# Kernel optimization log

Hardware: AMD Instinct MI355X
Metric: run time of the kernel (lower is better)

The kernel has to match this reference:

```python
import jax, jax.numpy as jnp
import numpy as np

NUM_PTS = 4
N_OFF = 4


def inverse_sigmoid(x, eps=1e-5):
    x = jnp.clip(x, 0.0, 1.0)
    return jnp.log(jnp.clip(x, eps, None) / jnp.clip(1.0 - x, eps, None))


def uniform_flat_indices(T, H, W, n):
    # torch: linspace(hop/2, D-1-hop/2, n).round().long(), meshed over (t,h,w)
    def ax(D):
        hop = D / n
        return jnp.round(jnp.linspace(hop / 2.0, D - 1.0 - hop / 2.0, n)).astype(jnp.int32)
    ti, hi, wi = ax(T), ax(H), ax(W)
    return ((ti[:, None, None] * H + hi[None, :, None]) * W + wi[None, None, :]).reshape(-1)


def _normalized_thw(idx, T, H, W):
    wn = (idx % W).astype(jnp.float32) / (W - 1)
    hn = ((idx // W) % H).astype(jnp.float32) / (H - 1)
    tn = (idx // (W * H)).astype(jnp.float32) / (T - 1)
    return jnp.stack([tn, hn, wn], axis=-1)


def grid_sample_3d(inp, grid):
    # Matches torch F.grid_sample 5D, bilinear, padding zeros, align_corners=False.
    # inp: (N,C,D,H,W); grid: (N,Do,Ho,Wo,3) with grid[...,0]=x->W, 1=y->H, 2=z->D
    N, C, D, H, W = inp.shape
    Do, Ho, Wo = grid.shape[1:4]
    P = Do * Ho * Wo
    g = grid.reshape(N, P, 3)
    ix = ((g[..., 0] + 1.0) * W - 1.0) * 0.5
    iy = ((g[..., 1] + 1.0) * H - 1.0) * 0.5
    iz = ((g[..., 2] + 1.0) * D - 1.0) * 0.5
    x0 = jnp.floor(ix); y0 = jnp.floor(iy); z0 = jnp.floor(iz)
    fx = ix - x0; fy = iy - y0; fz = iz - z0
    x0i = x0.astype(jnp.int32); y0i = y0.astype(jnp.int32); z0i = z0.astype(jnp.int32)
    inp_flat = inp.reshape(N, C, D * H * W)
    out = jnp.zeros((N, C, P), inp.dtype)
    for dz in (0, 1):
        for dy in (0, 1):
            for dx in (0, 1):
                xi = x0i + dx; yi = y0i + dy; zi = z0i + dz
                w = (fx if dx else 1.0 - fx) * (fy if dy else 1.0 - fy) * (fz if dz else 1.0 - fz)
                valid = (xi >= 0) & (xi < W) & (yi >= 0) & (yi < H) & (zi >= 0) & (zi < D)
                flat = (jnp.clip(zi, 0, D - 1) * H + jnp.clip(yi, 0, H - 1)) * W + jnp.clip(xi, 0, W - 1)
                vals = jnp.take_along_axis(inp_flat, jnp.broadcast_to(flat[:, None, :], (N, C, P)), axis=2)
                out = out + vals * (w * valid.astype(inp.dtype))[:, None, :]
    return out.reshape(N, C, Do, Ho, Wo)


def forward(features, pos, W1, b1, W2, b2, Wn, bn, Wl, bl, Woff, boff, Ww, bw, gamma, beta):
    B, C, T, H, Wd, L = features.shape
    THW = T * H * Wd
    No = N_OFF
    N = NUM_PTS ** 3
    d = C // No
    BLNo = B * L * No

    flat = uniform_flat_indices(T, H, Wd, NUM_PTS)                    # (N,)
    ind_pts = jnp.broadcast_to(flat[None, None, :], (B, L, N))

    feats_l = jnp.transpose(features, (0, 5, 2, 3, 4, 1)).reshape(B, L, THW, C)
    pos_l = jnp.transpose(pos, (0, 5, 2, 3, 4, 1)).reshape(B, L, THW, C)
    sampled_pts = feats_l[:, :, flat, :]                              # (B,L,N,C)
    sampled_pos = pos_l[:, :, flat, :]
    glob = jnp.transpose(jnp.mean(features, axis=(2, 3, 4)), (0, 2, 1))  # (B,L,C)
    glob = jnp.broadcast_to(glob[:, :, None, :], (B, L, N, C))

    off_src = jnp.concatenate([sampled_pts, sampled_pos, glob], axis=-1)
    off_src = jax.nn.relu(off_src @ W1 + b1)
    off_src = jax.nn.relu(off_src @ W2 + b2)                          # (B,L,N,C)

    nxt = off_src @ Wn + bn                                           # (B,L,N,3)
    w_l = jax.nn.softmax(off_src @ Wl + bl, axis=-1)                  # (B,L,N,L)

    osr = off_src.reshape(B, L, N, No, d).transpose(0, 1, 3, 2, 4).reshape(BLNo, N, d)
    offset = osr @ Woff + boff                                        # (BLNo,N,3)
    w_o = jax.nn.softmax(osr @ Ww + bw, axis=-1)[..., 1:]             # (BLNo,N,1)

    # --- build flow field: identity grid with sampled coords scattered in ---
    idx = jnp.broadcast_to(ind_pts[:, :, None, :], (B, L, No, N)).reshape(BLNo, N)
    thw = _normalized_thw(idx, T, H, Wd)
    samp = jax.nn.sigmoid(inverse_sigmoid(thw) + offset) * 2.0 - 1.0  # (BLNo,N,3)
    mesh = jnp.stack(jnp.meshgrid(jnp.linspace(-1.0, 1.0, T), jnp.linspace(-1.0, 1.0, H), jnp.linspace(-1.0, 1.0, Wd), indexing='ij'), axis=-1).reshape(THW, 3)
    base = jnp.broadcast_to(mesh[None], (BLNo, THW, 3))
    bI = jnp.arange(BLNo)[:, None]
    flow = base.at[bI, idx].set(samp).reshape(BLNo, T, H, Wd, 3)

    feats_rep = jnp.transpose(features, (0, 5, 1, 2, 3, 4))           # (B,L,C,T,H,W)
    feats_rep = jnp.broadcast_to(feats_rep[:, :, None], (B, L, No, C, T, H, Wd)).reshape(BLNo, C, T, H, Wd)
    sf = grid_sample_3d(feats_rep, flow)                              # (BLNo,C,T,H,W)
    sf = jnp.transpose(sf, (0, 2, 3, 4, 1))                           # (BLNo,T,H,W,C)

    wo_full = jnp.zeros((BLNo, THW, 1), features.dtype).at[bI, idx].set(w_o).reshape(BLNo, T, H, Wd, 1)
    wsf = (sf * wo_full).reshape(B, L, No, T, H, Wd, C).sum(axis=2)   # (B,L,T,H,W,C)
    feats2 = features + jnp.transpose(wsf, (0, 5, 2, 3, 4, 1))        # (B,C,T,H,W,L)

    # level weights scattered then summed over target-level axis l
    bI2 = jnp.arange(B)[:, None, None]
    lI2 = jnp.arange(L)[None, :, None]
    wl_full = jnp.zeros((B, L, THW, L), features.dtype).at[bI2, lI2, ind_pts].set(w_l)
    wl_sum = wl_full.sum(axis=-1).reshape(B, L, T, H, Wd)             # (B,L,T,H,W)
    feats3 = feats2 * jnp.transpose(wl_sum, (0, 2, 3, 4, 1))[:, None] # broadcast over C

    # LayerNorm over channel dim (transpose(1,-1) in torch)
    x = jnp.transpose(feats3, (0, 5, 2, 3, 4, 1))                     # (B,L,T,H,W,C)
    mu = jnp.mean(x, axis=-1, keepdims=True)
    var = jnp.var(x, axis=-1, keepdims=True)
    xn = (x - mu) * jax.lax.rsqrt(var + 1e-5) * gamma + beta
    feats_out = jnp.transpose(xn, (0, 5, 2, 3, 4, 1))

    # offset_adder -> next flattened indices
    thw2 = _normalized_thw(ind_pts, T, H, Wd)
    disp = jax.nn.sigmoid(inverse_sigmoid(thw2) + nxt)
    scale = jnp.array([T - 1, H - 1, Wd - 1], jnp.float32)
    di = jnp.round(disp * scale).astype(jnp.int32)
    next_ind = H * Wd * di[..., 0] + Wd * di[..., 1] + di[..., 2]
    return feats_out, next_ind


def setup_inputs():
    key = jax.random.key(0)
    ks = jax.random.split(key, 10)
    B, C, T, H, W, L = 1, 256, 8, 32, 32, 4
    s = 0.02
    d = C // N_OFF
    return {
        'features': jax.random.normal(ks[0], (B, C, T, H, W, L), jnp.float32),
        'pos': jax.random.normal(ks[1], (B, C, T, H, W, L), jnp.float32),
        'W1': jax.random.normal(ks[2], (3 * C, C), jnp.float32) * s,
        'b1': jnp.zeros((C,), jnp.float32),
        'W2': jax.random.normal(ks[3], (C, C), jnp.float32) * s,
        'b2': jnp.zeros((C,), jnp.float32),
        'Wn': jax.random.normal(ks[4], (C, 3), jnp.float32) * s,
        'bn': jnp.zeros((3,), jnp.float32),
        'Wl': jax.random.normal(ks[5], (C, L), jnp.float32) * s,
        'bl': jnp.zeros((L,), jnp.float32),
        'Woff': jax.random.normal(ks[6], (d, 3), jnp.float32) * s,
        'boff': jnp.zeros((3,), jnp.float32),
        'Ww': jax.random.normal(ks[7], (d, 2), jnp.float32) * s,
        'bw': jnp.zeros((2,), jnp.float32),
        'gamma': jnp.ones((C,), jnp.float32),
        'beta': jnp.zeros((C,), jnp.float32),
    }


def reference(features, pos, W1, b1, W2, b2, Wn, bn, Wl, bl, Woff, boff, Ww, bw, gamma, beta):
    return forward(features, pos, W1, b1, W2, b2, Wn, bn, Wl, bl, Woff, boff, Ww, bw, gamma, beta)
```

## Files before the change

kernel.cpp:

```cpp
#include <hip/hip_runtime.h>
#include <math.h>

#define CDIM 256
#define TDIM 8
#define HDIM 32
#define WDIM 32
#define LDIM 4
#define THW 8192
#define CSTR 32768
#define NS 64
#define OUT0_SIZE 8388608

__device__ __constant__ int c_ti[4] = {1, 3, 4, 6};
__device__ __constant__ int c_hw[4] = {4, 12, 19, 27};

__device__ __forceinline__ float sigm(float x) { return 1.f / (1.f + expf(-x)); }

__device__ __forceinline__ float wave_sum64(float x) {
#pragma unroll
    for (int s = 32; s > 0; s >>= 1) x += __shfl_xor(x, s, 64);
    return x;
}

__global__ void __launch_bounds__(256)
k_fill_part(const float* __restrict__ feat, const float* __restrict__ beta,
            float* __restrict__ out, float4* __restrict__ partF) {
    int c = blockIdx.x >> 3, part = blockIdx.x & 7;
    float bv = beta[c];
    float4 bf = make_float4(bv, bv, bv, bv);
    const float4* f = (const float4*)(feat + (size_t)c * CSTR) + part * 1024;
    float4* o = (float4*)(out + (size_t)c * CSTR) + part * 1024;
    float4 a = make_float4(0.f, 0.f, 0.f, 0.f);
#pragma unroll
    for (int it = 0; it < 4; ++it) {
        int i = it * 256 + threadIdx.x;
        float4 v = f[i];
        o[i] = bf;
        a.x += v.x; a.y += v.y; a.z += v.z; a.w += v.w;
    }
#pragma unroll
    for (int s = 32; s > 0; s >>= 1) {
        a.x += __shfl_xor(a.x, s, 64);
        a.y += __shfl_xor(a.y, s, 64);
        a.z += __shfl_xor(a.z, s, 64);
        a.w += __shfl_xor(a.w, s, 64);
    }
    __shared__ float4 sw[4];
    if ((threadIdx.x & 63) == 0) sw[threadIdx.x >> 6] = a;
    __syncthreads();
    if (threadIdx.x == 0) {
        float4 r;
        r.x = sw[0].x + sw[1].x + sw[2].x + sw[3].x;
        r.y = sw[0].y + sw[1].y + sw[2].y + sw[3].y;
        r.z = sw[0].z + sw[1].z + sw[2].z + sw[3].z;
        r.w = sw[0].w + sw[1].w + sw[2].w + sw[3].w;
        partF[blockIdx.x] = r;
    }
}

__global__ void __launch_bounds__(256)
k_gather(const float* __restrict__ feat, const float* __restrict__ pos,
         const float4* __restrict__ partF, float* __restrict__ in1T) {
    int k = blockIdx.x;
    int m = threadIdx.x;
    int l = m >> 6, n = m & 63;
    int sp = (c_ti[n >> 4] * HDIM + c_hw[(n >> 2) & 3]) * WDIM + c_hw[n & 3];
    float val;
    if (k < 256) {
        val = feat[(size_t)k * CSTR + sp * LDIM + l];
    } else if (k < 512) {
        val = pos[(size_t)(k - 256) * CSTR + sp * LDIM + l];
    } else {
        int c = k - 512;
        float s = 0.f;
#pragma unroll
        for (int p = 0; p < 8; ++p) {
            float4 v = partF[c * 8 + p];
            s += (l == 0) ? v.x : (l == 1) ? v.y : (l == 2) ? v.z : v.w;
        }
        val = s * (1.f / 8192.f);
    }
    in1T[(size_t)k * 256 + m] = val;
}

template <int KITER, int WRITE_T>
__global__ void __launch_bounds__(256)
k_gemm(const float* __restrict__ AT, const float* __restrict__ Wt,
       const float* __restrict__ bias, float* __restrict__ outp) {
    __shared__ float aLds[256 * 20];
    __shared__ float sAcc[256][33];
    int mt = blockIdx.x >> 4, jt = blockIdx.x & 15;
    int m0 = mt * 16, j0 = jt * 16;
    int t = threadIdx.x;
    int j8 = t & 7, kq = t >> 3;
    int j = j0 + j8 * 2;
    float acc0[16], acc1[16];
#pragma unroll
    for (int i = 0; i < 16; ++i) { acc0[i] = 0.f; acc1[i] = 0.f; }

    constexpr int NCHUNK = KITER / 8;
    for (int ch = 0; ch < NCHUNK; ++ch) {
        if (ch) __syncthreads();
#pragma unroll
        for (int i = 0; i < 4; ++i) {
            int idx = i * 256 + t;
            int k = idx >> 2, mq = idx & 3;
            *(float4*)(&aLds[k * 20 + mq * 4]) =
                *(const float4*)(AT + (size_t)(ch * 256 + k) * 256 + m0 + mq * 4);
        }
        __syncthreads();
#pragma unroll
        for (int kk2 = 0; kk2 < 8; ++kk2) {
            int kl = kq + (kk2 << 5);
            int kg = ch * 256 + kl;
            const float* ar = &aLds[kl * 20];
            float av[16];
            ((float4*)av)[0] = *(const float4*)(ar + 0);
            ((float4*)av)[1] = *(const float4*)(ar + 4);
            ((float4*)av)[2] = *(const float4*)(ar + 8);
            ((float4*)av)[3] = *(const float4*)(ar + 12);
            float2 w = *(const float2*)(Wt + (size_t)kg * 256 + j);
#pragma unroll
            for (int i = 0; i < 16; ++i) {
                acc0[i] = fmaf(av[i], w.x, acc0[i]);
                acc1[i] = fmaf(av[i], w.y, acc1[i]);
            }
        }
    }
    __syncthreads();
#pragma unroll
    for (int i = 0; i < 16; ++i) {
        sAcc[i * 16 + j8 * 2 + 0][kq] = acc0[i];
        sAcc[i * 16 + j8 * 2 + 1][kq] = acc1[i];
    }
    __syncthreads();
    int i = t >> 4, jj = t & 15;
    float v = bias[j0 + jj];
#pragma unroll
    for (int q = 0; q < 32; ++q) v += sAcc[t][q];
    v = fmaxf(v, 0.f);
    if (WRITE_T)
        outp[(size_t)(j0 + jj) * 256 + m0 + i] = v;
    else
        outp[(size_t)(m0 + i) * 256 + j0 + jj] = v;
}

__global__ void __launch_bounds__(512)
k_heads_sample(const float* __restrict__ feat, const float* __restrict__ osrc,
               const float* __restrict__ Wn, const float* __restrict__ bn,
               const float* __restrict__ Woff, const float* __restrict__ boff,
               const float* __restrict__ Ww, const float* __restrict__ bw,
               const float* __restrict__ gamma, const float* __restrict__ beta,
               float* __restrict__ out, float* __restrict__ next_out) {
    __shared__ float s_samp[4][3];
    __shared__ float s_wo[4];
    __shared__ float s_w[32];
    __shared__ int   s_o[32];
    __shared__ float red1[4], red2[4], redn[3][4];
    __shared__ float sPa[2][256];

    int m = blockIdx.x, l = m >> 6, n = m & 63;
    int t = threadIdx.x;
    int sp = (c_ti[n >> 4] * HDIM + c_hw[(n >> 2) & 3]) * WDIM + c_hw[n & 3];

    if (t < 256) {
        int j = t, o = j >> 6, r = j & 63;
        float v = osrc[(size_t)m * 256 + j];

        float pn0 = wave_sum64(v * Wn[j * 3 + 0]);
        float pn1 = wave_sum64(v * Wn[j * 3 + 1]);
        float pn2 = wave_sum64(v * Wn[j * 3 + 2]);
        if (r == 0) { redn[0][o] = pn0; redn[1][o] = pn1; redn[2][o] = pn2; }

        float po0 = wave_sum64(v * Woff[r * 3 + 0]);
        float po1 = wave_sum64(v * Woff[r * 3 + 1]);
        float po2 = wave_sum64(v * Woff[r * 3 + 2]);
        float z0  = wave_sum64(v * Ww[r * 2 + 0]);
        float z1  = wave_sum64(v * Ww[r * 2 + 1]);

        if (r == 0) {
            float tn = (float)c_ti[n >> 4] / 7.f;
            float hn = (float)c_hw[(n >> 2) & 3] / 31.f;
            float wn = (float)c_hw[n & 3] / 31.f;
            float lg0 = logf(tn / (1.f - tn));
            float lg1 = logf(hn / (1.f - hn));
            float lg2 = logf(wn / (1.f - wn));
            s_samp[o][0] = sigm(lg0 + po0 + boff[0]) * 2.f - 1.f;
            s_samp[o][1] = sigm(lg1 + po1 + boff[1]) * 2.f - 1.f;
            s_samp[o][2] = sigm(lg2 + po2 + boff[2]) * 2.f - 1.f;
            s_wo[o] = 1.f / (1.f + expf((z0 + bw[0]) - (z1 + bw[1])));
        }
    }
    __syncthreads();

    if (t == 0) {
        float tn = (float)c_ti[n >> 4] / 7.f;
        float hn = (float)c_hw[(n >> 2) & 3] / 31.f;
        float wn = (float)c_hw[n & 3] / 31.f;
        float lg0 = logf(tn / (1.f - tn));
        float lg1 = logf(hn / (1.f - hn));
        float lg2 = logf(wn / (1.f - wn));
        float t0 = redn[0][0] + redn[0][1] + redn[0][2] + redn[0][3];
        float t1 = redn[1][0] + redn[1][1] + redn[1][2] + redn[1][3];
        float t2 = redn[2][0] + redn[2][1] + redn[2][2] + redn[2][3];
        float d0 = rintf(sigm(lg0 + t0 + bn[0]) * 7.f);
        float d1 = rintf(sigm(lg1 + t1 + bn[1]) * 31.f);
        float d2 = rintf(sigm(lg2 + t2 + bn[2]) * 31.f);
        next_out[m] = 1024.f * d0 + 32.f * d1 + d2;
    }

    if (t < 4) {
        int oo = t;
        float wv = s_wo[oo];
        float g0 = s_samp[oo][0], g1 = s_samp[oo][1], g2 = s_samp[oo][2];
        float ix = ((g0 + 1.f) * 32.f - 1.f) * 0.5f;
        float iy = ((g1 + 1.f) * 32.f - 1.f) * 0.5f;
        float iz = ((g2 + 1.f) * 8.f  - 1.f) * 0.5f;
        float x0f = floorf(ix), y0f = floorf(iy), z0f = floorf(iz);
        float fx = ix - x0f, fy = iy - y0f, fz = iz - z0f;
        int x0 = (int)x0f, y0 = (int)y0f, z0 = (int)z0f;
#pragma unroll
        for (int k = 0; k < 8; ++k) {
            int dx = k & 1, dy = (k >> 1) & 1, dz = k >> 2;
            int xi = x0 + dx, yi = y0 + dy, zi = z0 + dz;
            float w = (dx ? fx : 1.f - fx) * (dy ? fy : 1.f - fy) * (dz ? fz : 1.f - fz);
            bool valid = (xi >= 0) && (xi < WDIM) && (yi >= 0) && (yi < HDIM) && (zi >= 0) && (zi < TDIM);
            int xc = min(max(xi, 0), WDIM - 1);
            int yc = min(max(yi, 0), HDIM - 1);
            int zc = min(max(zi, 0), TDIM - 1);
            s_w[oo * 8 + k] = valid ? w * wv : 0.f;
            s_o[oo * 8 + k] = ((zc * HDIM + yc) * WDIM + xc) * LDIM + l;
        }
    }
    __syncthreads();

    {
        int c = t & 255, h = t >> 8;
        const float* fc = feat + (size_t)c * CSTR;
        float vals[16];
        int base = h * 16;
#pragma unroll
        for (int k = 0; k < 16; ++k) vals[k] = fc[s_o[base + k]];
        float acc = (h == 0) ? fc[sp * LDIM + l] : 0.f;
#pragma unroll
        for (int k = 0; k < 16; ++k) acc += s_w[base + k] * vals[k];
        sPa[h][c] = acc;
    }
    __syncthreads();

    float accf = 0.f;
    if (t < 256) {
        accf = sPa[0][t] + sPa[1][t];
        float s1 = accf, s2 = accf * accf;
#pragma unroll
        for (int d = 32; d > 0; d >>= 1) { s1 += __shfl_xor(s1, d, 64); s2 += __shfl_xor(s2, d, 64); }
        int wid = t >> 6;
        if ((t & 63) == 0) { red1[wid] = s1; red2[wid] = s2; }
    }
    __syncthreads();
    if (t < 256) {
        int c = t;
        float tot  = red1[0] + red1[1] + red1[2] + red1[3];
        float totq = red2[0] + red2[1] + red2[2] + red2[3];
        float mu = tot * (1.f / 256.f);
        float var = fmaxf(totq * (1.f / 256.f) - mu * mu, 0.f);
        float y = (accf - mu) * rsqrtf(var + 1e-5f) * gamma[c] + beta[c];
        out[(size_t)c * CSTR + sp * LDIM + l] = y;
    }
}

extern "C" void kernel_launch(void* const* d_in, const int* in_sizes, int n_in,
                              void* d_out, int out_size, void* d_ws, size_t ws_size,
                              hipStream_t stream) {
    const float* feat = (const float*)d_in[0];
    const float* pos  = (const float*)d_in[1];
    const float* W1   = (const float*)d_in[2];
    const float* b1   = (const float*)d_in[3];
    const float* W2   = (const float*)d_in[4];
    const float* b2   = (const float*)d_in[5];
    const float* Wn   = (const float*)d_in[6];
    const float* bn   = (const float*)d_in[7];
    const float* Woff = (const float*)d_in[10];
    const float* boff = (const float*)d_in[11];
    const float* Ww   = (const float*)d_in[12];
    const float* bw   = (const float*)d_in[13];
    const float* gamma= (const float*)d_in[14];
    const float* beta = (const float*)d_in[15];
    float* out = (float*)d_out;
    float* next_out = out + OUT0_SIZE;

    float* ws    = (float*)d_ws;
    float4* partF= (float4*)ws;
    float* in1T  = ws + 8192;
    float* h1T   = in1T + 196608;
    float* osrc  = h1T + 65536;

    k_fill_part<<<2048, 256, 0, stream>>>(feat, beta, out, partF);
    k_gather<<<768, 256, 0, stream>>>(feat, pos, partF, in1T);
    k_gemm<24, 1><<<256, 256, 0, stream>>>(in1T, W1, b1, h1T);
    k_gemm<8, 0><<<256, 256, 0, stream>>>(h1T, W2, b2, osrc);
    k_heads_sample<<<256, 512, 0, stream>>>(feat, osrc, Wn, bn, Woff, boff, Ww, bw,
                                            gamma, beta, out, next_out);
}
```

Measured before the change: 153.7 us.

## Fuse gather, both MLP GEMMs and heads into one per-query kernel

Replaces the gather, two tiled GEMM kernels and the heads/sample kernel with a single kernel where each block handles one query row. The block gathers its input vector into shared memory and runs both matrix-vector products against W1 and W2 directly, then continues into the heads. This removes three launches and the workspace round trips between them. In exchange, each of the 256 blocks reads the full W1 and W2 from global memory (relying on L2), and the GEMMs become matrix-vector work with less reuse.

```diff
diff --git a/kernel.cpp b/kernel.cpp
--- a/kernel.cpp
+++ b/kernel.cpp
@@ -58,100 +58,20 @@
     }
 }
 
-__global__ void __launch_bounds__(256)
-k_gather(const float* __restrict__ feat, const float* __restrict__ pos,
-         const float4* __restrict__ partF, float* __restrict__ in1T) {
-    int k = blockIdx.x;
-    int m = threadIdx.x;
-    int l = m >> 6, n = m & 63;
-    int sp = (c_ti[n >> 4] * HDIM + c_hw[(n >> 2) & 3]) * WDIM + c_hw[n & 3];
-    float val;
-    if (k < 256) {
-        val = feat[(size_t)k * CSTR + sp * LDIM + l];
-    } else if (k < 512) {
-        val = pos[(size_t)(k - 256) * CSTR + sp * LDIM + l];
-    } else {
-        int c = k - 512;
-        float s = 0.f;
-#pragma unroll
-        for (int p = 0; p < 8; ++p) {
-            float4 v = partF[c * 8 + p];
-            s += (l == 0) ? v.x : (l == 1) ? v.y : (l == 2) ? v.z : v.w;
-        }
-        val = s * (1.f / 8192.f);
-    }
-    in1T[(size_t)k * 256 + m] = val;
-}
-
-template <int KITER, int WRITE_T>
-__global__ void __launch_bounds__(256)
-k_gemm(const float* __restrict__ AT, const float* __restrict__ Wt,
-       const float* __restrict__ bias, float* __restrict__ outp) {
-    __shared__ float aLds[256 * 20];
-    __shared__ float sAcc[256][33];
-    int mt = blockIdx.x >> 4, jt = blockIdx.x & 15;
-    int m0 = mt * 16, j0 = jt * 16;
-    int t = threadIdx.x;
-    int j8 = t & 7, kq = t >> 3;
-    int j = j0 + j8 * 2;
-    float acc0[16], acc1[16];
-#pragma unroll
-    for (int i = 0; i < 16; ++i) { acc0[i] = 0.f; acc1[i] = 0.f; }
-
-    constexpr int NCHUNK = KITER / 8;
-    for (int ch = 0; ch < NCHUNK; ++ch) {
-        if (ch) __syncthreads();
-#pragma unroll
-        for (int i = 0; i < 4; ++i) {
-            int idx = i * 256 + t;
-            int k = idx >> 2, mq = idx & 3;
-            *(float4*)(&aLds[k * 20 + mq * 4]) =
-                *(const float4*)(AT + (size_t)(ch * 256 + k) * 256 + m0 + mq * 4);
-        }
-        __syncthreads();
-#pragma unroll
-        for (int kk2 = 0; kk2 < 8; ++kk2) {
-            int kl = kq + (kk2 << 5);
-            int kg = ch * 256 + kl;
-            const float* ar = &aLds[kl * 20];
-            float av[16];
-            ((float4*)av)[0] = *(const float4*)(ar + 0);
-            ((float4*)av)[1] = *(const float4*)(ar + 4);
-            ((float4*)av)[2] = *(const float4*)(ar + 8);
-            ((float4*)av)[3] = *(const float4*)(ar + 12);
-            float2 w = *(const float2*)(Wt + (size_t)kg * 256 + j);
-#pragma unroll
-            for (int i = 0; i < 16; ++i) {
-                acc0[i] = fmaf(av[i], w.x, acc0[i]);
-                acc1[i] = fmaf(av[i], w.y, acc1[i]);
-            }
-        }
-    }
-    __syncthreads();
-#pragma unroll
-    for (int i = 0; i < 16; ++i) {
-        sAcc[i * 16 + j8 * 2 + 0][kq] = acc0[i];
-        sAcc[i * 16 + j8 * 2 + 1][kq] = acc1[i];
-    }
-    __syncthreads();
-    int i = t >> 4, jj = t & 15;
-    float v = bias[j0 + jj];
-#pragma unroll
-    for (int q = 0; q < 32; ++q) v += sAcc[t][q];
-    v = fmaxf(v, 0.f);
-    if (WRITE_T)
-        outp[(size_t)(j0 + jj) * 256 + m0 + i] = v;
-    else
-        outp[(size_t)(m0 + i) * 256 + j0 + jj] = v;
-}
-
 __global__ void __launch_bounds__(512)
-k_heads_sample(const float* __restrict__ feat, const float* __restrict__ osrc,
-               const float* __restrict__ Wn, const float* __restrict__ bn,
-               const float* __restrict__ Woff, const float* __restrict__ boff,
-               const float* __restrict__ Ww, const float* __restrict__ bw,
-               const float* __restrict__ gamma, const float* __restrict__ beta,
-               float* __restrict__ out, float* __restrict__ next_out) {
+k_rest(const float* __restrict__ feat, const float* __restrict__ pos,
+       const float4* __restrict__ partF,
+       const float* __restrict__ W1, const float* __restrict__ b1,
+       const float* __restrict__ W2, const float* __restrict__ b2,
+       const float* __restrict__ Wn, const float* __restrict__ bn,
+       const float* __restrict__ Woff, const float* __restrict__ boff,
+       const float* __restrict__ Ww, const float* __restrict__ bw,
+       const float* __restrict__ gamma, const float* __restrict__ beta,
+       float* __restrict__ out, float* __restrict__ next_out) {
+    __shared__ float sA[768];
+    __shared__ float sRed[8][256];
+    __shared__ float sH[256];
+    __shared__ float sO[256];
     __shared__ float s_samp[4][3];
     __shared__ float s_wo[4];
     __shared__ float s_w[32];
@@ -159,13 +79,74 @@
     __shared__ float red1[4], red2[4], redn[3][4];
     __shared__ float sPa[2][256];
 
-    int m = blockIdx.x, l = m >> 6, n = m & 63;
-    int t = threadIdx.x;
-    int sp = (c_ti[n >> 4] * HDIM + c_hw[(n >> 2) & 3]) * WDIM + c_hw[n & 3];
+    const int m = blockIdx.x, l = m >> 6, n = m & 63;
+    const int t = threadIdx.x;
+    const int sp = (c_ti[n >> 4] * HDIM + c_hw[(n >> 2) & 3]) * WDIM + c_hw[n & 3];
+
+    {
+        int c = t & 255;
+        if (t < 256) {
+            sA[c] = feat[(size_t)c * CSTR + sp * LDIM + l];
+            float s = 0.f;
+#pragma unroll
+            for (int p = 0; p < 8; ++p) {
+                float4 v = partF[c * 8 + p];
+                s += (l == 0) ? v.x : (l == 1) ? v.y : (l == 2) ? v.z : v.w;
+            }
+            sA[512 + c] = s * (1.f / 8192.f);
+        } else {
+            sA[256 + c] = pos[(size_t)c * CSTR + sp * LDIM + l];
+        }
+    }
+    __syncthreads();
+
+    {
+        int j4 = t & 63, kq = t >> 6;
+        const float4* Wp = (const float4*)W1 + (size_t)(kq * 96) * 64 + j4;
+        float ax = 0.f, ay = 0.f, az = 0.f, aw = 0.f;
+#pragma unroll 8
+        for (int kk = 0; kk < 96; ++kk) {
+            float a = sA[kq * 96 + kk];
+            float4 w = Wp[(size_t)kk * 64];
+            ax = fmaf(a, w.x, ax); ay = fmaf(a, w.y, ay);
+            az = fmaf(a, w.z, az); aw = fmaf(a, w.w, aw);
+        }
+        *(float4*)&sRed[kq][j4 * 4] = make_float4(ax, ay, az, aw);
+    }
+    __syncthreads();
+    if (t < 256) {
+        float v = b1[t];
+#pragma unroll
+        for (int q = 0; q < 8; ++q) v += sRed[q][t];
+        sH[t] = fmaxf(v, 0.f);
+    }
+    __syncthreads();
+
+    {
+        int j4 = t & 63, kq = t >> 6;
+        const float4* Wp = (const float4*)W2 + (size_t)(kq * 32) * 64 + j4;
+        float ax = 0.f, ay = 0.f, az = 0.f, aw = 0.f;
+#pragma unroll 8
+        for (int kk = 0; kk < 32; ++kk) {
+            float a = sH[kq * 32 + kk];
+            float4 w = Wp[(size_t)kk * 64];
+            ax = fmaf(a, w.x, ax); ay = fmaf(a, w.y, ay);
+            az = fmaf(a, w.z, az); aw = fmaf(a, w.w, aw);
+        }
+        *(float4*)&sRed[kq][j4 * 4] = make_float4(ax, ay, az, aw);
+    }
+    __syncthreads();
+    if (t < 256) {
+        float v = b2[t];
+#pragma unroll
+        for (int q = 0; q < 8; ++q) v += sRed[q][t];
+        sO[t] = fmaxf(v, 0.f);
+    }
+    __syncthreads();
 
     if (t < 256) {
         int j = t, o = j >> 6, r = j & 63;
-        float v = osrc[(size_t)m * 256 + j];
+        float v = sO[j];
 
         float pn0 = wave_sum64(v * Wn[j * 3 + 0]);
         float pn1 = wave_sum64(v * Wn[j * 3 + 1]);
@@ -289,16 +270,9 @@
     float* out = (float*)d_out;
     float* next_out = out + OUT0_SIZE;
 
-    float* ws    = (float*)d_ws;
-    float4* partF= (float4*)ws;
-    float* in1T  = ws + 8192;
-    float* h1T   = in1T + 196608;
-    float* osrc  = h1T + 65536;
+    float4* partF = (float4*)d_ws;
 
     k_fill_part<<<2048, 256, 0, stream>>>(feat, beta, out, partF);
-    k_gather<<<768, 256, 0, stream>>>(feat, pos, partF, in1T);
-    k_gemm<24, 1><<<256, 256, 0, stream>>>(in1T, W1, b1, h1T);
-    k_gemm<8, 0><<<256, 256, 0, stream>>>(h1T, W2, b2, osrc);
-    k_heads_sample<<<256, 512, 0, stream>>>(feat, osrc, Wn, bn, Woff, boff, Ww, bw,
-                                            gamma, beta, out, next_out);
-}
+    k_rest<<<256, 512, 0, stream>>>(feat, pos, partF, W1, b1, W2, b2, Wn, bn,
+                                    Woff, boff, Ww, bw, gamma, beta, out, next_out);
+}
```

New measurement: 154.5 us. No clear change (+0.5%).
